# Kernel optimization log

Measured on AMD Instinct MI355X. Metric: run time of the kernel, lower is better.

Reference implementation:

```python
import jax, jax.numpy as jnp
import numpy as np

D = 768
H = 8
DH = D // H
SCALE = DH ** -0.5


def layer_norm(x, g, b, eps=1e-5):
    mu = jnp.mean(x, axis=-1, keepdims=True)
    var = jnp.var(x, axis=-1, keepdims=True)
    return (x - mu) * jax.lax.rsqrt(var + eps) * g + b


def setup_inputs() -> dict:
    key = jax.random.key(0)
    ks = jax.random.split(key, 8)
    B, N = 8, 1024
    s = lambda fan_in: 1.0 / np.sqrt(fan_in)
    return {
        "x": jax.random.normal(ks[0], (B, N, D), jnp.float32),
        "w_qkv": jax.random.normal(ks[1], (D, 3 * D), jnp.float32) * s(D),
        "w_o": jax.random.normal(ks[2], (D, D), jnp.float32) * s(D),
        "b_o": jnp.zeros((D,), jnp.float32),
        "w1": jax.random.normal(ks[3], (D, 4 * D), jnp.float32) * s(D),
        "b1": jnp.zeros((4 * D,), jnp.float32),
        "w2": jax.random.normal(ks[4], (4 * D, D), jnp.float32) * s(4 * D),
        "b2": jnp.zeros((D,), jnp.float32),
        "g1": jnp.ones((D,), jnp.float32), "be1": jnp.zeros((D,), jnp.float32),
        "gm": jnp.ones((D,), jnp.float32), "bm": jnp.zeros((D,), jnp.float32),
        "g3": jnp.ones((D,), jnp.float32), "be3": jnp.zeros((D,), jnp.float32),
    }


def reference(x, w_qkv, w_o, b_o, w1, b1, w2, b2, g1, be1, gm, bm, g3, be3):
    B, N, _ = x.shape
    # --- attention branch (pre-norm) ---
    h = layer_norm(x, g1, be1)
    qkv = h @ w_qkv                                   # (B,N,3D)
    qkv = qkv.reshape(B, N, 3, H, DH).transpose(2, 0, 3, 1, 4)  # (3,B,H,N,Dh)
    q, k, v = qkv[0], qkv[1], qkv[2]
    att = jax.nn.softmax(jnp.einsum('bhnd,bhmd->bhnm', q, k) * SCALE, axis=-1)
    o = jnp.einsum('bhnm,bhmd->bhnd', att, v)         # (B,H,N,Dh)
    # faithful to original: reshape WITHOUT transposing heads back
    o = o.reshape(B, N, D)
    o = o @ w_o + b_o
    x = o + x
    # --- MLP branch (has its own pre-norm; GELU after BOTH linears; dropout off) ---
    h = layer_norm(x, gm, bm)
    h = jax.nn.gelu(h @ w1 + b1, approximate=False)
    h = jax.nn.gelu(h @ w2 + b2, approximate=False)
    x = h + x
    return layer_norm(x, g3, be3)
```

## Files before the change

kernel.cpp:

```cpp
#include <hip/hip_runtime.h>
#include <cmath>
#include <cstdint>

typedef __bf16 bf16;
typedef __bf16 bf16x8 __attribute__((ext_vector_type(8)));
typedef __bf16 bf16x4 __attribute__((ext_vector_type(4)));
typedef float  f32x4  __attribute__((ext_vector_type(4)));

#define M_TOK 8192
#define SCALE_ 0.10206207261596575f

__device__ __forceinline__ void gld_lds16(const void* g, void* l) {
  __builtin_amdgcn_global_load_lds(
      (__attribute__((address_space(1))) void*)(uintptr_t)g,
      (__attribute__((address_space(3))) void*)(uintptr_t)l,
      16, 0, 0);
}

__device__ __forceinline__ float gelu_f(float x) {
  float u = x * (0.7978845608f + 0.0356774081f * x * x);
  float t = 1.0f - 2.0f / (__expf(2.0f * u) + 1.0f);
  return 0.5f * x * (1.0f + t);
}

__global__ __launch_bounds__(256) void make_frags_kernel(
    const float* __restrict__ w_qkv, const float* __restrict__ w_o,
    const float* __restrict__ w1, const float* __restrict__ w2,
    bf16* __restrict__ fqkv, bf16* __restrict__ fwo, bf16* __restrict__ fw1,
    bf16* __restrict__ fw2) {
  int chunk = blockIdx.x * 4 + (threadIdx.x >> 6);
  int lane = threadIdx.x & 63;
  const float* src;
  bf16* dst;
  int K, N, base;
  if (chunk < 3456) {
    src = w_qkv; dst = fqkv; K = 768; N = 2304; base = 0;
  } else if (chunk < 4608) {
    src = w_o; dst = fwo; K = 768; N = 768; base = 3456;
  } else if (chunk < 9216) {
    src = w1; dst = fw1; K = 768; N = 3072; base = 4608;
  } else {
    src = w2; dst = fw2; K = 3072; N = 768; base = 9216;
  }
  int lid = chunk - base;
  int kc = K / 32;
  int n16 = lid / kc, c = lid - n16 * kc;
  int lr = lane & 15, qd = lane >> 4;
  int n = n16 * 16 + lr;
  int k0 = c * 32 + qd * 8;
  bf16x8 v;
#pragma unroll
  for (int e = 0; e < 8; e++) v[e] = (bf16)src[(size_t)(k0 + e) * N + n];
  *(bf16x8*)&dst[(size_t)lid * 512 + lane * 8] = v;
}

__global__ __launch_bounds__(256) void ln_kernel(
    const float* __restrict__ x, const float* __restrict__ g,
    const float* __restrict__ b, bf16* __restrict__ ob) {
  int w = threadIdx.x >> 6, lane = threadIdx.x & 63;
  size_t row = (size_t)blockIdx.x * 4 + w;
  const float* xr = x + row * 768;
  float4 v[3];
  float s = 0.f, sq = 0.f;
#pragma unroll
  for (int k = 0; k < 3; k++) {
    v[k] = *(const float4*)(xr + (k * 64 + lane) * 4);
    s += v[k].x + v[k].y + v[k].z + v[k].w;
    sq += v[k].x * v[k].x + v[k].y * v[k].y + v[k].z * v[k].z + v[k].w * v[k].w;
  }
#pragma unroll
  for (int off = 32; off >= 1; off >>= 1) {
    s += __shfl_xor(s, off);
    sq += __shfl_xor(sq, off);
  }
  float mean = s * (1.f / 768.f);
  float rstd = rsqrtf(sq * (1.f / 768.f) - mean * mean + 1e-5f);
#pragma unroll
  for (int k = 0; k < 3; k++) {
    int c = (k * 64 + lane) * 4;
    float4 gg = *(const float4*)(g + c);
    float4 bb = *(const float4*)(b + c);
    bf16x4 pk = {(bf16)((v[k].x - mean) * rstd * gg.x + bb.x),
                 (bf16)((v[k].y - mean) * rstd * gg.y + bb.y),
                 (bf16)((v[k].z - mean) * rstd * gg.z + bb.z),
                 (bf16)((v[k].w - mean) * rstd * gg.w + bb.w)};
    *(bf16x4*)(ob + row * 768 + c) = pk;
  }
}

__global__ __launch_bounds__(256) void ln2_reduce_kernel(
    const bf16* __restrict__ p, const float* __restrict__ bo,
    const float* __restrict__ xres, const float* __restrict__ g,
    const float* __restrict__ b, bf16* __restrict__ x2,
    bf16* __restrict__ h2) {
  int w = threadIdx.x >> 6, lane = threadIdx.x & 63;
  size_t row = (size_t)blockIdx.x * 4 + w;
  const bf16* p0 = p + row * 768;
  const bf16* p1 = p0 + (size_t)M_TOK * 768;
  const float* xr = xres + row * 768;
  float4 v[3];
  float s = 0.f, sq = 0.f;
#pragma unroll
  for (int k = 0; k < 3; k++) {
    int c = (k * 64 + lane) * 4;
    bf16x4 a0 = *(const bf16x4*)(p0 + c);
    bf16x4 a1 = *(const bf16x4*)(p1 + c);
    float4 bb = *(const float4*)(bo + c);
    float4 rr = *(const float4*)(xr + c);
    v[k].x = (float)a0[0] + (float)a1[0] + bb.x + rr.x;
    v[k].y = (float)a0[1] + (float)a1[1] + bb.y + rr.y;
    v[k].z = (float)a0[2] + (float)a1[2] + bb.z + rr.z;
    v[k].w = (float)a0[3] + (float)a1[3] + bb.w + rr.w;
    bf16x4 xo = {(bf16)v[k].x, (bf16)v[k].y, (bf16)v[k].z, (bf16)v[k].w};
    *(bf16x4*)(x2 + row * 768 + c) = xo;
    s += v[k].x + v[k].y + v[k].z + v[k].w;
    sq += v[k].x * v[k].x + v[k].y * v[k].y + v[k].z * v[k].z + v[k].w * v[k].w;
  }
#pragma unroll
  for (int off = 32; off >= 1; off >>= 1) {
    s += __shfl_xor(s, off);
    sq += __shfl_xor(sq, off);
  }
  float mean = s * (1.f / 768.f);
  float rstd = rsqrtf(sq * (1.f / 768.f) - mean * mean + 1e-5f);
#pragma unroll
  for (int k = 0; k < 3; k++) {
    int c = (k * 64 + lane) * 4;
    float4 gg = *(const float4*)(g + c);
    float4 bb = *(const float4*)(b + c);
    bf16x4 pk = {(bf16)((v[k].x - mean) * rstd * gg.x + bb.x),
                 (bf16)((v[k].y - mean) * rstd * gg.y + bb.y),
                 (bf16)((v[k].z - mean) * rstd * gg.z + bb.z),
                 (bf16)((v[k].w - mean) * rstd * gg.w + bb.w)};
    *(bf16x4*)(h2 + row * 768 + c) = pk;
  }
}

__global__ __launch_bounds__(256) void ln3_reduce_kernel(
    const bf16* __restrict__ p, const float* __restrict__ b2,
    const bf16* __restrict__ x2, const float* __restrict__ g,
    const float* __restrict__ b, float* __restrict__ out) {
  int w = threadIdx.x >> 6, lane = threadIdx.x & 63;
  size_t row = (size_t)blockIdx.x * 4 + w;
  const bf16* p0 = p + row * 768;
  const bf16* p1 = p0 + (size_t)M_TOK * 768;
  const bf16* xr = x2 + row * 768;
  float4 v[3];
  float s = 0.f, sq = 0.f;
#pragma unroll
  for (int k = 0; k < 3; k++) {
    int c = (k * 64 + lane) * 4;
    bf16x4 a0 = *(const bf16x4*)(p0 + c);
    bf16x4 a1 = *(const bf16x4*)(p1 + c);
    float4 bb = *(const float4*)(b2 + c);
    bf16x4 rr = *(const bf16x4*)(xr + c);
    v[k].x = gelu_f((float)a0[0] + (float)a1[0] + bb.x) + (float)rr[0];
    v[k].y = gelu_f((float)a0[1] + (float)a1[1] + bb.y) + (float)rr[1];
    v[k].z = gelu_f((float)a0[2] + (float)a1[2] + bb.z) + (float)rr[2];
    v[k].w = gelu_f((float)a0[3] + (float)a1[3] + bb.w) + (float)rr[3];
    s += v[k].x + v[k].y + v[k].z + v[k].w;
    sq += v[k].x * v[k].x + v[k].y * v[k].y + v[k].z * v[k].z + v[k].w * v[k].w;
  }
#pragma unroll
  for (int off = 32; off >= 1; off >>= 1) {
    s += __shfl_xor(s, off);
    sq += __shfl_xor(sq, off);
  }
  float mean = s * (1.f / 768.f);
  float rstd = rsqrtf(sq * (1.f / 768.f) - mean * mean + 1e-5f);
#pragma unroll
  for (int k = 0; k < 3; k++) {
    int c = (k * 64 + lane) * 4;
    float4 gg = *(const float4*)(g + c);
    float4 bb = *(const float4*)(b + c);
    float4 ov = {(v[k].x - mean) * rstd * gg.x + bb.x,
                 (v[k].y - mean) * rstd * gg.y + bb.y,
                 (v[k].z - mean) * rstd * gg.z + bb.z,
                 (v[k].w - mean) * rstd * gg.w + bb.w};
    *(float4*)(out + row * 768 + c) = ov;
  }
}

template <int EPI, int LDA, int KTOT, int KSL, int NN>
__global__ __launch_bounds__(256, 3) void gemm128_kernel(
    const bf16* __restrict__ A, const bf16* __restrict__ Bf,
    const float* __restrict__ bias, bf16* __restrict__ outb,
    bf16* __restrict__ qo, bf16* __restrict__ ko, bf16* __restrict__ vto) {
  constexpr int KCg = KTOT / 32;
  constexpr int NT = KSL / 32;
  __shared__ __align__(16) bf16 smem[3][8192];
  int tid = threadIdx.x;
  int w = tid >> 6, l = tid & 63;
  int qd = l >> 4, lr = l & 15;
  int id2 = blockIdx.y * gridDim.x + blockIdx.x;
  int xcd = id2 & 7;
  int slot = id2 >> 3;
  int Mg = gridDim.x >> 3;
  int mt = xcd * Mg + (slot % Mg);
  int ntl = slot / Mg;
  int bm0 = mt * 128, bn0 = ntl * 128;
  int kb = blockIdx.z * KSL;
  int wm = (w >> 1) * 64, wn = (w & 1) * 64;
  int wnl = (w & 1) * 4;

  const bf16* pA = A + (size_t)(bm0 + w * 32 + (l >> 2)) * LDA + kb +
                   (((l & 3) ^ ((l >> 3) & 3)) * 8);
  const bf16* pB =
      Bf + ((size_t)((bn0 >> 4) + w * 2) * KCg + (kb >> 5)) * 512 + l * 8;

  auto STG = [&](int t, int b) {
    char* dA = (char*)smem[b] + w * 2048;
    char* dB = (char*)smem[b] + 8192 + w * 2048;
    gld_lds16(pA + t * 32, dA);
    gld_lds16(pA + t * 32 + (size_t)16 * LDA, dA + 1024);
    gld_lds16(pB + (size_t)t * 512, dB);
    gld_lds16(pB + (size_t)KCg * 512 + (size_t)t * 512, dB + 1024);
  };
  auto LDF = [&](int b, bf16x8* af, bf16x8* bv) {
    const bf16* Ab = smem[b];
    const bf16* Bb = smem[b] + 4096;
#pragma unroll
    for (int i = 0; i < 4; ++i) {
      int r = wm + i * 16 + lr;
      af[i] = *(const bf16x8*)(Ab + r * 32 + ((qd ^ ((lr >> 1) & 3)) * 8));
    }
#pragma unroll
    for (int j = 0; j < 4; ++j)
      bv[j] = *(const bf16x8*)(Bb + (wnl + j) * 512 + l * 8);
  };

  f32x4 acc[4][4] = {};

  STG(0, 0);
  STG(1, 1);
  asm volatile("s_waitcnt vmcnt(4)" ::: "memory");
  __builtin_amdgcn_sched_barrier(0);
  __builtin_amdgcn_s_barrier();

#pragma unroll 1
  for (int t3 = 0; t3 < NT; t3 += 3) {
#pragma unroll
    for (int u = 0; u < 3; ++u) {
      const int t = t3 + u;
      const bool st = (t + 2) < NT;
      if (st) STG(t + 2, (u + 2) % 3);
      __builtin_amdgcn_sched_barrier(0);
      bf16x8 af[4], bv[4];
      LDF(u, af, bv);
      asm volatile("s_waitcnt lgkmcnt(0)" ::: "memory");
      __builtin_amdgcn_sched_barrier(0);
      __builtin_amdgcn_s_setprio(1);
#pragma unroll
      for (int i = 0; i < 4; ++i)
#pragma unroll
        for (int j = 0; j < 4; ++j)
          acc[i][j] = __builtin_amdgcn_mfma_f32_16x16x32_bf16(
              af[i], bv[j], acc[i][j], 0, 0, 0);
      __builtin_amdgcn_s_setprio(0);
      if (t + 1 < NT) {
        if (st) asm volatile("s_waitcnt vmcnt(4)" ::: "memory");
        else    asm volatile("s_waitcnt vmcnt(0)" ::: "memory");
        __builtin_amdgcn_sched_barrier(0);
        __builtin_amdgcn_s_barrier();
      }
    }
  }

  bf16* outbs = (EPI == 5) ? outb + (size_t)blockIdx.z * M_TOK * NN : outb;

#pragma unroll
  for (int i = 0; i < 4; i++) {
#pragma unroll
    for (int j = 0; j < 4; j++) {
      if (EPI == 4) {
        int colt = bn0 + wn + j * 16;
        int which = colt / 768;
        int rem = colt - which * 768;
        int h = rem / 96;
        int dhb = rem - h * 96;
        int row0 = bm0 + wm + i * 16 + qd * 4;
        int b = row0 >> 10, n0 = row0 & 1023;
        int bh = b * 8 + h;
        if (which == 2) {
          bf16x4 pk = {(bf16)acc[i][j][0], (bf16)acc[i][j][1],
                       (bf16)acc[i][j][2], (bf16)acc[i][j][3]};
          *(bf16x4*)(vto + ((size_t)(bh * 96 + dhb + lr)) * 1024 + n0) = pk;
        } else if (which == 0) {
#pragma unroll
          for (int r = 0; r < 4; r++)
            qo[((size_t)bh * 1024 + n0 + r) * 96 + dhb + lr] =
                (bf16)(acc[i][j][r] * SCALE_);
        } else {
#pragma unroll
          for (int r = 0; r < 4; r++)
            ko[((size_t)bh * 1024 + n0 + r) * 96 + dhb + lr] =
                (bf16)acc[i][j][r];
        }
      } else {
#pragma unroll
        for (int r = 0; r < 4; r++) {
          int row = bm0 + wm + i * 16 + qd * 4 + r;
          int col = bn0 + wn + j * 16 + lr;
          size_t o = (size_t)row * NN + col;
          float v = acc[i][j][r];
          if (EPI == 2) {
            outbs[o] = (bf16)gelu_f(v + bias[col]);
          } else {
            outbs[o] = (bf16)v;
          }
        }
      }
    }
  }
}

__global__ __launch_bounds__(256) void attn_kernel(
    const bf16* __restrict__ qb, const bf16* __restrict__ kb,
    const bf16* __restrict__ vtb, bf16* __restrict__ operm) {
  __shared__ __align__(16) bf16 Ks[2][64 * 104];
  __shared__ __align__(16) bf16 Vs[2][96 * 72];
  __shared__ __align__(16) bf16 Ps[128 * 72];
  int t = threadIdx.x;
  int w = t >> 6, lane = t & 63;
  int qd = lane >> 4, lr = lane & 15;
  int bh = blockIdx.x, nt0 = blockIdx.y * 128;
  int bq = bh >> 3, hh = bh & 7;

  const bf16* kgb = kb + (size_t)bh * 1024 * 96;
  const bf16* vgb = vtb + (size_t)bh * 96 * 1024;

  bf16x8 kreg[3], vreg[3];
#pragma unroll
  for (int it = 0; it < 3; it++) {
    int idx = it * 256 + t;
    kreg[it] = *(const bf16x8*)(kgb + (idx / 12) * 96 + (idx % 12) * 8);
    vreg[it] = *(const bf16x8*)(vgb + (size_t)(idx >> 3) * 1024 + (idx & 7) * 8);
  }

  const bf16* qg = qb + ((size_t)bh * 1024 + nt0 + w * 32) * 96;
  bf16x8 afq[2][3];
#pragma unroll
  for (int i = 0; i < 2; i++)
#pragma unroll
    for (int ks = 0; ks < 3; ks++)
      afq[i][ks] = *(const bf16x8*)(qg + (i * 16 + lr) * 96 + ks * 32 + qd * 8);

  f32x4 oacc[2][6] = {};
  float lst[2][4] = {};

  int cur = 0;
  for (int kt = 0; kt < 16; kt++) {
#pragma unroll
    for (int it = 0; it < 3; it++) {
      int idx = it * 256 + t;
      *(bf16x8*)&Ks[cur][(idx / 12) * 104 + (idx % 12) * 8] = kreg[it];
      *(bf16x8*)&Vs[cur][(idx >> 3) * 72 + (idx & 7) * 8] = vreg[it];
    }
    if (kt < 15) {
      const bf16* kg = kgb + (size_t)(kt + 1) * 64 * 96;
      const bf16* vg = vgb + (kt + 1) * 64;
#pragma unroll
      for (int it = 0; it < 3; it++) {
        int idx = it * 256 + t;
        kreg[it] = *(const bf16x8*)(kg + (idx / 12) * 96 + (idx % 12) * 8);
        vreg[it] =
            *(const bf16x8*)(vg + (size_t)(idx >> 3) * 1024 + (idx & 7) * 8);
      }
    }
    __syncthreads();

    f32x4 sacc[2][4] = {};
#pragma unroll
    for (int ks = 0; ks < 3; ks++) {
      bf16x8 bk[4];
#pragma unroll
      for (int jn = 0; jn < 4; jn++)
        bk[jn] =
            *(const bf16x8*)&Ks[cur][(jn * 16 + lr) * 104 + ks * 32 + qd * 8];
#pragma unroll
      for (int i = 0; i < 2; i++)
#pragma unroll
        for (int jn = 0; jn < 4; jn++)
          sacc[i][jn] = __builtin_amdgcn_mfma_f32_16x16x32_bf16(
              afq[i][ks], bk[jn], sacc[i][jn], 0, 0, 0);
    }

#pragma unroll
    for (int i = 0; i < 2; i++)
#pragma unroll
      for (int jn = 0; jn < 4; jn++)
#pragma unroll
        for (int r = 0; r < 4; r++) {
          float p = __expf(sacc[i][jn][r]);
          lst[i][r] += p;
          Ps[(w * 32 + i * 16 + qd * 4 + r) * 72 + jn * 16 + lr] = (bf16)p;
        }

#pragma unroll
    for (int ks = 0; ks < 2; ks++) {
      bf16x8 ap[2];
#pragma unroll
      for (int i = 0; i < 2; i++)
        ap[i] =
            *(const bf16x8*)&Ps[(w * 32 + i * 16 + lr) * 72 + ks * 32 + qd * 8];
#pragma unroll
      for (int jn = 0; jn < 6; jn++) {
        bf16x8 bv =
            *(const bf16x8*)&Vs[cur][(jn * 16 + lr) * 72 + ks * 32 + qd * 8];
#pragma unroll
        for (int i = 0; i < 2; i++)
          oacc[i][jn] = __builtin_amdgcn_mfma_f32_16x16x32_bf16(
              ap[i], bv, oacc[i][jn], 0, 0, 0);
      }
    }
    cur ^= 1;
  }

#pragma unroll
  for (int i = 0; i < 2; i++)
#pragma unroll
    for (int r = 0; r < 4; r++) {
#pragma unroll
      for (int off = 1; off < 16; off <<= 1)
        lst[i][r] += __shfl_xor(lst[i][r], off);
    }

#pragma unroll
  for (int i = 0; i < 2; i++) {
#pragma unroll
    for (int r = 0; r < 4; r++) {
      float inv = 1.0f / lst[i][r];
      int n = nt0 + w * 32 + i * 16 + qd * 4 + r;
      size_t rowo = (size_t)bq * 1024 + hh * 128 + (n >> 3);
      int colb = 96 * (n & 7);
#pragma unroll
      for (int jn = 0; jn < 6; jn++)
        operm[rowo * 768 + colb + jn * 16 + lr] =
            (bf16)(oacc[i][jn][r] * inv);
    }
  }
}

extern "C" void kernel_launch(void* const* d_in, const int* in_sizes, int n_in,
                              void* d_out, int out_size, void* d_ws,
                              size_t ws_size, hipStream_t stream) {
  const float* x = (const float*)d_in[0];
  const float* w_qkv = (const float*)d_in[1];
  const float* w_o = (const float*)d_in[2];
  const float* b_o = (const float*)d_in[3];
  const float* w1 = (const float*)d_in[4];
  const float* b1 = (const float*)d_in[5];
  const float* w2 = (const float*)d_in[6];
  const float* b2 = (const float*)d_in[7];
  const float* g1 = (const float*)d_in[8];
  const float* be1 = (const float*)d_in[9];
  const float* gm = (const float*)d_in[10];
  const float* bm = (const float*)d_in[11];
  const float* g3 = (const float*)d_in[12];
  const float* be3 = (const float*)d_in[13];

  char* ws = (char*)d_ws;
  size_t off = 0;
  auto alloc = [&](size_t bytes) {
    char* p = ws + off;
    off += (bytes + 255) & ~(size_t)255;
    return p;
  };
  const size_t SZ_TOK_BF = (size_t)M_TOK * 768 * 2;
  bf16* fqkv = (bf16*)alloc((size_t)2304 * 768 * 2);
  bf16* fwo = (bf16*)alloc((size_t)768 * 768 * 2);
  bf16* fw1 = (bf16*)alloc((size_t)3072 * 768 * 2);
  bf16* fw2 = (bf16*)alloc((size_t)768 * 3072 * 2);
  bf16* hA = (bf16*)alloc(SZ_TOK_BF);
  bf16* qb = (bf16*)alloc(SZ_TOK_BF);
  bf16* kbuf = (bf16*)alloc(SZ_TOK_BF);
  bf16* vtb = (bf16*)alloc(SZ_TOK_BF);
  bf16* x2 = (bf16*)alloc(SZ_TOK_BF);
  char* G = alloc((size_t)M_TOK * 3072 * 2);
  bf16* operm = hA;
  bf16* h2 = hA;
  bf16* pWo = (bf16*)G;
  bf16* a1 = (bf16*)G;
  bf16* pW2 = hA;

  make_frags_kernel<<<3456, 256, 0, stream>>>(w_qkv, w_o, w1, w2, fqkv, fwo,
                                              fw1, fw2);

  ln_kernel<<<M_TOK / 4, 256, 0, stream>>>(x, g1, be1, hA);

  gemm128_kernel<4, 768, 768, 768, 2304><<<dim3(64, 18), 256, 0, stream>>>(
      hA, fqkv, nullptr, nullptr, qb, kbuf, vtb);

  attn_kernel<<<dim3(64, 8), 256, 0, stream>>>(qb, kbuf, vtb, operm);

  gemm128_kernel<5, 768, 768, 384, 768><<<dim3(64, 6, 2), 256, 0, stream>>>(
      operm, fwo, nullptr, pWo, nullptr, nullptr, nullptr);

  ln2_reduce_kernel<<<M_TOK / 4, 256, 0, stream>>>(pWo, b_o, x, gm, bm, x2, h2);

  gemm128_kernel<2, 768, 768, 768, 3072><<<dim3(64, 24), 256, 0, stream>>>(
      h2, fw1, b1, a1, nullptr, nullptr, nullptr);

  gemm128_kernel<5, 3072, 3072, 1536, 768><<<dim3(64, 6, 2), 256, 0, stream>>>(
      a1, fw2, nullptr, pW2, nullptr, nullptr, nullptr);

  ln3_reduce_kernel<<<M_TOK / 4, 256, 0, stream>>>(pW2, b2, x2, g3, be3,
                                                   (float*)d_out);
}
```

Baseline: 321.0 us.

## Add 256x256-tile 8-wave GEMM with ping-pong LDS pipeline for QKV and MLP

Adds a new GEMM kernel that uses 256x256 output tiles, 512 threads, a 64-wide K step and double-buffered 128KB LDS. Global-to-LDS staging is interleaved with MFMA sub-phases, and each sub-phase is separated by barriers. The QKV, MLP-up and MLP-down GEMMs move to this kernel, while the 128-tile kernel is kept only for the output projection. Larger tiles raise arithmetic intensity and cut redundant global loads. In exchange the grids are smaller (288/384/192 blocks at one block per CU), which risks tail effects and lower occupancy, and the many barriers add synchronisation cost.

```diff
diff --git a/kernel.cpp b/kernel.cpp
--- a/kernel.cpp
+++ b/kernel.cpp
@@ -9,6 +9,7 @@
 
 #define M_TOK 8192
 #define SCALE_ 0.10206207261596575f
+#define SB0 __builtin_amdgcn_sched_barrier(0)
 
 __device__ __forceinline__ void gld_lds16(const void* g, void* l) {
   __builtin_amdgcn_global_load_lds(
@@ -178,6 +179,196 @@
                  (v[k].z - mean) * rstd * gg.z + bb.z,
                  (v[k].w - mean) * rstd * gg.w + bb.w};
     *(float4*)(out + row * 768 + c) = ov;
+  }
+}
+
+template <int EPI, int LDA, int KTOT, int KSL, int NN>
+__global__ __launch_bounds__(512, 1) void gemm256_kernel(
+    const bf16* __restrict__ A, const bf16* __restrict__ Bf,
+    const float* __restrict__ bias, bf16* __restrict__ outb,
+    bf16* __restrict__ qo, bf16* __restrict__ ko, bf16* __restrict__ vto) {
+  constexpr int KCg = KTOT / 32;
+  constexpr int NT = KSL / 64;
+  constexpr int NI = NT / 2;
+  __shared__ __align__(16) bf16 smem[2][32768];
+  int tid = threadIdx.x;
+  int w = tid >> 6, l = tid & 63;
+  int qd = l >> 4, lr = l & 15;
+  int bm0 = blockIdx.x * 256, bn0 = blockIdx.y * 256;
+  int kb = blockIdx.z * KSL;
+  int wm = (w >> 2) * 128;
+  int wn = (w & 3) * 64;
+  int wnl = (w & 3) * 4;
+
+  const bf16* pA = A + (size_t)(bm0 + w * 32 + (l >> 2)) * LDA + kb +
+                   (((l & 3) ^ ((l >> 3) & 3)) * 8);
+  const bf16* pB =
+      Bf + ((size_t)((bn0 >> 4) + 2 * w) * KCg + (kb >> 5)) * 512 + l * 8;
+
+  auto STG_A = [&](int t, int kc, bf16* buf) {
+    const bf16* s = pA + t * 64 + kc * 32;
+    char* d = (char*)buf + kc * 16384 + w * 2048;
+    gld_lds16(s, d);
+    gld_lds16(s + (size_t)16 * LDA, d + 1024);
+  };
+  auto STG_B = [&](int t, int kc, bf16* buf) {
+    const bf16* s = pB + (size_t)(t * 2 + kc) * 512;
+    char* d = (char*)buf + 32768 + kc * 16384 + w * 2048;
+    gld_lds16(s, d);
+    gld_lds16(s + (size_t)KCg * 512, d + 1024);
+  };
+  auto LD_A4 = [&](const bf16* buf, int kc, int i0, bf16x8* af) {
+#pragma unroll
+    for (int i = 0; i < 4; ++i) {
+      int r = wm + (i0 + i) * 16 + lr;
+      af[i] = *(const bf16x8*)(buf + kc * 8192 + r * 32 +
+                               ((qd ^ ((lr >> 1) & 3)) * 8));
+    }
+  };
+  auto LD_B4 = [&](const bf16* buf, int kc, bf16x8* bv) {
+#pragma unroll
+    for (int j = 0; j < 4; ++j)
+      bv[j] = *(const bf16x8*)(buf + 16384 + kc * 8192 + (wnl + j) * 512 +
+                               l * 8);
+  };
+
+  f32x4 acc[8][4] = {};
+  auto MM = [&](bf16x8* af, bf16x8* bv, int i0) {
+#pragma unroll
+    for (int i = 0; i < 4; ++i)
+#pragma unroll
+      for (int j = 0; j < 4; ++j)
+        acc[i0 + i][j] = __builtin_amdgcn_mfma_f32_16x16x32_bf16(
+            af[i], bv[j], acc[i0 + i][j], 0, 0, 0);
+  };
+
+  bf16* b0 = smem[0];
+  bf16* b1 = smem[1];
+
+  STG_B(0, 0, b0); STG_A(0, 0, b0); STG_B(0, 1, b0); STG_A(0, 1, b0);
+  STG_B(1, 0, b1); STG_A(1, 0, b1); STG_B(1, 1, b1);
+  asm volatile("s_waitcnt vmcnt(6)" ::: "memory");
+  SB0;
+  __builtin_amdgcn_s_barrier();
+  SB0;
+
+  bf16x8 af[4], bv[4];
+
+#pragma unroll 1
+  for (int it = 0; it < NI; ++it) {
+    const int T = 2 * it;
+    const bool st = (it + 1 < NI);
+
+    SB0; LD_B4(b0, 0, bv); LD_A4(b0, 0, 0, af); SB0;
+    STG_A(T + 1, 1, b1);
+    SB0; __builtin_amdgcn_s_barrier();
+    asm volatile("s_waitcnt lgkmcnt(0)" ::: "memory"); SB0;
+    __builtin_amdgcn_s_setprio(1); MM(af, bv, 0); __builtin_amdgcn_s_setprio(0);
+    SB0; __builtin_amdgcn_s_barrier();
+
+    SB0; LD_A4(b0, 0, 4, af); SB0;
+    if (st) STG_B(T + 2, 0, b0);
+    SB0; __builtin_amdgcn_s_barrier();
+    asm volatile("s_waitcnt lgkmcnt(0)" ::: "memory"); SB0;
+    __builtin_amdgcn_s_setprio(1); MM(af, bv, 4); __builtin_amdgcn_s_setprio(0);
+    SB0; __builtin_amdgcn_s_barrier();
+
+    SB0; LD_B4(b0, 1, bv); LD_A4(b0, 1, 0, af); SB0;
+    if (st) STG_A(T + 2, 0, b0);
+    SB0; __builtin_amdgcn_s_barrier();
+    asm volatile("s_waitcnt lgkmcnt(0)" ::: "memory"); SB0;
+    __builtin_amdgcn_s_setprio(1); MM(af, bv, 0); __builtin_amdgcn_s_setprio(0);
+    SB0; __builtin_amdgcn_s_barrier();
+
+    SB0; LD_A4(b0, 1, 4, af); SB0;
+    if (st) STG_B(T + 2, 1, b0);
+    SB0; __builtin_amdgcn_s_barrier();
+    asm volatile("s_waitcnt lgkmcnt(0)" ::: "memory"); SB0;
+    __builtin_amdgcn_s_setprio(1); MM(af, bv, 4); __builtin_amdgcn_s_setprio(0);
+    SB0;
+    if (st) asm volatile("s_waitcnt vmcnt(6)" ::: "memory");
+    else    asm volatile("s_waitcnt vmcnt(0)" ::: "memory");
+    SB0; __builtin_amdgcn_s_barrier();
+
+    SB0; LD_B4(b1, 0, bv); LD_A4(b1, 0, 0, af); SB0;
+    if (st) STG_A(T + 2, 1, b0);
+    SB0; __builtin_amdgcn_s_barrier();
+    asm volatile("s_waitcnt lgkmcnt(0)" ::: "memory"); SB0;
+    __builtin_amdgcn_s_setprio(1); MM(af, bv, 0); __builtin_amdgcn_s_setprio(0);
+    SB0; __builtin_amdgcn_s_barrier();
+
+    SB0; LD_A4(b1, 0, 4, af); SB0;
+    if (st) STG_B(T + 3, 0, b1);
+    SB0; __builtin_amdgcn_s_barrier();
+    asm volatile("s_waitcnt lgkmcnt(0)" ::: "memory"); SB0;
+    __builtin_amdgcn_s_setprio(1); MM(af, bv, 4); __builtin_amdgcn_s_setprio(0);
+    SB0; __builtin_amdgcn_s_barrier();
+
+    SB0; LD_B4(b1, 1, bv); LD_A4(b1, 1, 0, af); SB0;
+    if (st) STG_A(T + 3, 0, b1);
+    SB0; __builtin_amdgcn_s_barrier();
+    asm volatile("s_waitcnt lgkmcnt(0)" ::: "memory"); SB0;
+    __builtin_amdgcn_s_setprio(1); MM(af, bv, 0); __builtin_amdgcn_s_setprio(0);
+    SB0; __builtin_amdgcn_s_barrier();
+
+    SB0; LD_A4(b1, 1, 4, af); SB0;
+    if (st) STG_B(T + 3, 1, b1);
+    SB0; __builtin_amdgcn_s_barrier();
+    asm volatile("s_waitcnt lgkmcnt(0)" ::: "memory"); SB0;
+    __builtin_amdgcn_s_setprio(1); MM(af, bv, 4); __builtin_amdgcn_s_setprio(0);
+    SB0;
+    if (st) {
+      asm volatile("s_waitcnt vmcnt(6)" ::: "memory");
+      SB0;
+      __builtin_amdgcn_s_barrier();
+    }
+  }
+
+  bf16* outbs = (EPI == 5) ? outb + (size_t)blockIdx.z * M_TOK * NN : outb;
+
+#pragma unroll
+  for (int i = 0; i < 8; i++) {
+#pragma unroll
+    for (int j = 0; j < 4; j++) {
+      if (EPI == 4) {
+        int colt = bn0 + wn + j * 16;
+        int which = colt / 768;
+        int rem = colt - which * 768;
+        int h = rem / 96;
+        int dhb = rem - h * 96;
+        int row0 = bm0 + wm + i * 16 + qd * 4;
+        int b = row0 >> 10, n0 = row0 & 1023;
+        int bh = b * 8 + h;
+        if (which == 2) {
+          bf16x4 pk = {(bf16)acc[i][j][0], (bf16)acc[i][j][1],
+                       (bf16)acc[i][j][2], (bf16)acc[i][j][3]};
+          *(bf16x4*)(vto + ((size_t)(bh * 96 + dhb + lr)) * 1024 + n0) = pk;
+        } else if (which == 0) {
+#pragma unroll
+          for (int r = 0; r < 4; r++)
+            qo[((size_t)bh * 1024 + n0 + r) * 96 + dhb + lr] =
+                (bf16)(acc[i][j][r] * SCALE_);
+        } else {
+#pragma unroll
+          for (int r = 0; r < 4; r++)
+            ko[((size_t)bh * 1024 + n0 + r) * 96 + dhb + lr] =
+                (bf16)acc[i][j][r];
+        }
+      } else {
+#pragma unroll
+        for (int r = 0; r < 4; r++) {
+          int row = bm0 + wm + i * 16 + qd * 4 + r;
+          int col = bn0 + wn + j * 16 + lr;
+          size_t o = (size_t)row * NN + col;
+          float v = acc[i][j][r];
+          if (EPI == 2) {
+            outbs[o] = (bf16)gelu_f(v + bias[col]);
+          } else {
+            outbs[o] = (bf16)v;
+          }
+        }
+      }
+    }
   }
 }
 
@@ -234,7 +425,7 @@
   STG(0, 0);
   STG(1, 1);
   asm volatile("s_waitcnt vmcnt(4)" ::: "memory");
-  __builtin_amdgcn_sched_barrier(0);
+  SB0;
   __builtin_amdgcn_s_barrier();
 
 #pragma unroll 1
@@ -244,11 +435,11 @@
       const int t = t3 + u;
       const bool st = (t + 2) < NT;
       if (st) STG(t + 2, (u + 2) % 3);
-      __builtin_amdgcn_sched_barrier(0);
+      SB0;
       bf16x8 af[4], bv[4];
       LDF(u, af, bv);
       asm volatile("s_waitcnt lgkmcnt(0)" ::: "memory");
-      __builtin_amdgcn_sched_barrier(0);
+      SB0;
       __builtin_amdgcn_s_setprio(1);
 #pragma unroll
       for (int i = 0; i < 4; ++i)
@@ -260,7 +451,7 @@
       if (t + 1 < NT) {
         if (st) asm volatile("s_waitcnt vmcnt(4)" ::: "memory");
         else    asm volatile("s_waitcnt vmcnt(0)" ::: "memory");
-        __builtin_amdgcn_sched_barrier(0);
+        SB0;
         __builtin_amdgcn_s_barrier();
       }
     }
@@ -272,42 +463,16 @@
   for (int i = 0; i < 4; i++) {
 #pragma unroll
     for (int j = 0; j < 4; j++) {
-      if (EPI == 4) {
-        int colt = bn0 + wn + j * 16;
-        int which = colt / 768;
-        int rem = colt - which * 768;
-        int h = rem / 96;
-        int dhb = rem - h * 96;
-        int row0 = bm0 + wm + i * 16 + qd * 4;
-        int b = row0 >> 10, n0 = row0 & 1023;
-        int bh = b * 8 + h;
-        if (which == 2) {
-          bf16x4 pk = {(bf16)acc[i][j][0], (bf16)acc[i][j][1],
-                       (bf16)acc[i][j][2], (bf16)acc[i][j][3]};
-          *(bf16x4*)(vto + ((size_t)(bh * 96 + dhb + lr)) * 1024 + n0) = pk;
-        } else if (which == 0) {
-#pragma unroll
-          for (int r = 0; r < 4; r++)
-            qo[((size_t)bh * 1024 + n0 + r) * 96 + dhb + lr] =
-                (bf16)(acc[i][j][r] * SCALE_);
+#pragma unroll
+      for (int r = 0; r < 4; r++) {
+        int row = bm0 + wm + i * 16 + qd * 4 + r;
+        int col = bn0 + wn + j * 16 + lr;
+        size_t o = (size_t)row * NN + col;
+        float v = acc[i][j][r];
+        if (EPI == 2) {
+          outbs[o] = (bf16)gelu_f(v + bias[col]);
         } else {
-#pragma unroll
-          for (int r = 0; r < 4; r++)
-            ko[((size_t)bh * 1024 + n0 + r) * 96 + dhb + lr] =
-                (bf16)acc[i][j][r];
-        }
-      } else {
-#pragma unroll
-        for (int r = 0; r < 4; r++) {
-          int row = bm0 + wm + i * 16 + qd * 4 + r;
-          int col = bn0 + wn + j * 16 + lr;
-          size_t o = (size_t)row * NN + col;
-          float v = acc[i][j][r];
-          if (EPI == 2) {
-            outbs[o] = (bf16)gelu_f(v + bias[col]);
-          } else {
-            outbs[o] = (bf16)v;
-          }
+          outbs[o] = (bf16)v;
         }
       }
     }
@@ -488,7 +653,7 @@
 
   ln_kernel<<<M_TOK / 4, 256, 0, stream>>>(x, g1, be1, hA);
 
-  gemm128_kernel<4, 768, 768, 768, 2304><<<dim3(64, 18), 256, 0, stream>>>(
+  gemm256_kernel<4, 768, 768, 768, 2304><<<dim3(32, 9), 512, 0, stream>>>(
       hA, fqkv, nullptr, nullptr, qb, kbuf, vtb);
 
   attn_kernel<<<dim3(64, 8), 256, 0, stream>>>(qb, kbuf, vtb, operm);
@@ -498,10 +663,10 @@
 
   ln2_reduce_kernel<<<M_TOK / 4, 256, 0, stream>>>(pWo, b_o, x, gm, bm, x2, h2);
 
-  gemm128_kernel<2, 768, 768, 768, 3072><<<dim3(64, 24), 256, 0, stream>>>(
+  gemm256_kernel<2, 768, 768, 768, 3072><<<dim3(32, 12), 512, 0, stream>>>(
       h2, fw1, b1, a1, nullptr, nullptr, nullptr);
 
-  gemm128_kernel<5, 3072, 3072, 1536, 768><<<dim3(64, 6, 2), 256, 0, stream>>>(
+  gemm256_kernel<5, 3072, 3072, 1536, 768><<<dim3(32, 3, 2), 512, 0, stream>>>(
       a1, fw2, nullptr, pW2, nullptr, nullptr, nullptr);
 
   ln3_reduce_kernel<<<M_TOK / 4, 256, 0, stream>>>(pW2, b2, x2, g3, be3,
```

Result: slower. 360.5 us (+12.3%).

## Fuse output projection, residual and LayerNorm into attention kernel epilogue

Applied to the files above, without the earlier changes.

The attention kernel now stages its normalized output for 16 permuted token rows in LDS. It multiplies them by the W_o fragments directly from global memory, then adds bias and residual and computes the MLP pre-norm, writing x2 and h2. This removes the split-K Wo GEMM, the partial-sum round trip and the separate LN2 reduce kernel. It also XOR-swizzles the P tile in LDS to reduce bank conflicts. In exchange each attention block streams all of W_o from global/L2 with no LDS reuse, which lengthens the attention kernel and may lower its occupancy.

```diff
diff --git a/kernel.cpp b/kernel.cpp
--- a/kernel.cpp
+++ b/kernel.cpp
@@ -9,6 +9,7 @@
 
 #define M_TOK 8192
 #define SCALE_ 0.10206207261596575f
+#define SB0 __builtin_amdgcn_sched_barrier(0)
 
 __device__ __forceinline__ void gld_lds16(const void* g, void* l) {
   __builtin_amdgcn_global_load_lds(
@@ -85,54 +86,6 @@
                  (bf16)((v[k].z - mean) * rstd * gg.z + bb.z),
                  (bf16)((v[k].w - mean) * rstd * gg.w + bb.w)};
     *(bf16x4*)(ob + row * 768 + c) = pk;
-  }
-}
-
-__global__ __launch_bounds__(256) void ln2_reduce_kernel(
-    const bf16* __restrict__ p, const float* __restrict__ bo,
-    const float* __restrict__ xres, const float* __restrict__ g,
-    const float* __restrict__ b, bf16* __restrict__ x2,
-    bf16* __restrict__ h2) {
-  int w = threadIdx.x >> 6, lane = threadIdx.x & 63;
-  size_t row = (size_t)blockIdx.x * 4 + w;
-  const bf16* p0 = p + row * 768;
-  const bf16* p1 = p0 + (size_t)M_TOK * 768;
-  const float* xr = xres + row * 768;
-  float4 v[3];
-  float s = 0.f, sq = 0.f;
-#pragma unroll
-  for (int k = 0; k < 3; k++) {
-    int c = (k * 64 + lane) * 4;
-    bf16x4 a0 = *(const bf16x4*)(p0 + c);
-    bf16x4 a1 = *(const bf16x4*)(p1 + c);
-    float4 bb = *(const float4*)(bo + c);
-    float4 rr = *(const float4*)(xr + c);
-    v[k].x = (float)a0[0] + (float)a1[0] + bb.x + rr.x;
-    v[k].y = (float)a0[1] + (float)a1[1] + bb.y + rr.y;
-    v[k].z = (float)a0[2] + (float)a1[2] + bb.z + rr.z;
-    v[k].w = (float)a0[3] + (float)a1[3] + bb.w + rr.w;
-    bf16x4 xo = {(bf16)v[k].x, (bf16)v[k].y, (bf16)v[k].z, (bf16)v[k].w};
-    *(bf16x4*)(x2 + row * 768 + c) = xo;
-    s += v[k].x + v[k].y + v[k].z + v[k].w;
-    sq += v[k].x * v[k].x + v[k].y * v[k].y + v[k].z * v[k].z + v[k].w * v[k].w;
-  }
-#pragma unroll
-  for (int off = 32; off >= 1; off >>= 1) {
-    s += __shfl_xor(s, off);
-    sq += __shfl_xor(sq, off);
-  }
-  float mean = s * (1.f / 768.f);
-  float rstd = rsqrtf(sq * (1.f / 768.f) - mean * mean + 1e-5f);
-#pragma unroll
-  for (int k = 0; k < 3; k++) {
-    int c = (k * 64 + lane) * 4;
-    float4 gg = *(const float4*)(g + c);
-    float4 bb = *(const float4*)(b + c);
-    bf16x4 pk = {(bf16)((v[k].x - mean) * rstd * gg.x + bb.x),
-                 (bf16)((v[k].y - mean) * rstd * gg.y + bb.y),
-                 (bf16)((v[k].z - mean) * rstd * gg.z + bb.z),
-                 (bf16)((v[k].w - mean) * rstd * gg.w + bb.w)};
-    *(bf16x4*)(h2 + row * 768 + c) = pk;
   }
 }
 
@@ -234,7 +187,7 @@
   STG(0, 0);
   STG(1, 1);
   asm volatile("s_waitcnt vmcnt(4)" ::: "memory");
-  __builtin_amdgcn_sched_barrier(0);
+  SB0;
   __builtin_amdgcn_s_barrier();
 
 #pragma unroll 1
@@ -244,11 +197,11 @@
       const int t = t3 + u;
       const bool st = (t + 2) < NT;
       if (st) STG(t + 2, (u + 2) % 3);
-      __builtin_amdgcn_sched_barrier(0);
+      SB0;
       bf16x8 af[4], bv[4];
       LDF(u, af, bv);
       asm volatile("s_waitcnt lgkmcnt(0)" ::: "memory");
-      __builtin_amdgcn_sched_barrier(0);
+      SB0;
       __builtin_amdgcn_s_setprio(1);
 #pragma unroll
       for (int i = 0; i < 4; ++i)
@@ -260,7 +213,7 @@
       if (t + 1 < NT) {
         if (st) asm volatile("s_waitcnt vmcnt(4)" ::: "memory");
         else    asm volatile("s_waitcnt vmcnt(0)" ::: "memory");
-        __builtin_amdgcn_sched_barrier(0);
+        SB0;
         __builtin_amdgcn_s_barrier();
       }
     }
@@ -316,7 +269,10 @@
 
 __global__ __launch_bounds__(256) void attn_kernel(
     const bf16* __restrict__ qb, const bf16* __restrict__ kb,
-    const bf16* __restrict__ vtb, bf16* __restrict__ operm) {
+    const bf16* __restrict__ vtb, const bf16* __restrict__ fwo,
+    const float* __restrict__ bo, const float* __restrict__ xres,
+    const float* __restrict__ gm, const float* __restrict__ bm,
+    bf16* __restrict__ x2o, bf16* __restrict__ h2o) {
   __shared__ __align__(16) bf16 Ks[2][64 * 104];
   __shared__ __align__(16) bf16 Vs[2][96 * 72];
   __shared__ __align__(16) bf16 Ps[128 * 72];
@@ -393,7 +349,8 @@
         for (int r = 0; r < 4; r++) {
           float p = __expf(sacc[i][jn][r]);
           lst[i][r] += p;
-          Ps[(w * 32 + i * 16 + qd * 4 + r) * 72 + jn * 16 + lr] = (bf16)p;
+          Ps[(w * 32 + i * 16 + qd * 4 + r) * 72 + ((jn ^ qd) * 16 + lr)] =
+              (bf16)p;
         }
 
 #pragma unroll
@@ -401,8 +358,9 @@
       bf16x8 ap[2];
 #pragma unroll
       for (int i = 0; i < 2; i++)
-        ap[i] =
-            *(const bf16x8*)&Ps[(w * 32 + i * 16 + lr) * 72 + ks * 32 + qd * 8];
+        ap[i] = *(const bf16x8*)&Ps[(w * 32 + i * 16 + lr) * 72 +
+                                    ((ks * 32 + qd * 8) ^
+                                     (((lr >> 2) & 3) * 16))];
 #pragma unroll
       for (int jn = 0; jn < 6; jn++) {
         bf16x8 bv =
@@ -425,18 +383,89 @@
         lst[i][r] += __shfl_xor(lst[i][r], off);
     }
 
+  bf16* Po = (bf16*)&Ks[0][0];
+  float* red = (float*)&Vs[0][0];
+  int Rbase = bq * 1024 + hh * 128 + (nt0 >> 3);
+
+  __syncthreads();
 #pragma unroll
   for (int i = 0; i < 2; i++) {
 #pragma unroll
     for (int r = 0; r < 4; r++) {
       float inv = 1.0f / lst[i][r];
-      int n = nt0 + w * 32 + i * 16 + qd * 4 + r;
-      size_t rowo = (size_t)bq * 1024 + hh * 128 + (n >> 3);
-      int colb = 96 * (n & 7);
+      int nn = i * 16 + qd * 4 + r;
+      int rloc = w * 4 + (nn >> 3);
+      int colb = 96 * (nn & 7);
 #pragma unroll
       for (int jn = 0; jn < 6; jn++)
-        operm[rowo * 768 + colb + jn * 16 + lr] =
-            (bf16)(oacc[i][jn][r] * inv);
+        Po[rloc * 784 + colb + jn * 16 + lr] = (bf16)(oacc[i][jn][r] * inv);
+    }
+  }
+  __syncthreads();
+
+  f32x4 ya[12] = {};
+#pragma unroll 1
+  for (int kc = 0; kc < 24; ++kc) {
+    bf16x8 a = *(const bf16x8*)&Po[lr * 784 + kc * 32 + qd * 8];
+    const bf16* bp = fwo + ((size_t)(w * 12) * 24 + kc) * 512 + lane * 8;
+#pragma unroll
+    for (int j = 0; j < 12; ++j)
+      ya[j] = __builtin_amdgcn_mfma_f32_16x16x32_bf16(
+          a, *(const bf16x8*)(bp + (size_t)j * 12288), ya[j], 0, 0, 0);
+  }
+
+  float s4[4] = {}, q4[4] = {};
+#pragma unroll
+  for (int j = 0; j < 12; ++j) {
+    int col = (w * 12 + j) * 16 + lr;
+    float bcol = bo[col];
+#pragma unroll
+    for (int rr = 0; rr < 4; ++rr) {
+      size_t R = (size_t)(Rbase + qd * 4 + rr);
+      float tv = ya[j][rr] + bcol + xres[R * 768 + col];
+      ya[j][rr] = tv;
+      s4[rr] += tv;
+      q4[rr] += tv * tv;
+    }
+  }
+#pragma unroll
+  for (int rr = 0; rr < 4; ++rr) {
+#pragma unroll
+    for (int off = 1; off < 16; off <<= 1) {
+      s4[rr] += __shfl_xor(s4[rr], off);
+      q4[rr] += __shfl_xor(q4[rr], off);
+    }
+  }
+  if (lr == 0) {
+#pragma unroll
+    for (int rr = 0; rr < 4; ++rr) {
+      red[(qd * 4 + rr) * 8 + w * 2] = s4[rr];
+      red[(qd * 4 + rr) * 8 + w * 2 + 1] = q4[rr];
+    }
+  }
+  __syncthreads();
+  float mean[4], rstd[4];
+#pragma unroll
+  for (int rr = 0; rr < 4; ++rr) {
+    float ss = 0.f, qq = 0.f;
+#pragma unroll
+    for (int wv = 0; wv < 4; ++wv) {
+      ss += red[(qd * 4 + rr) * 8 + wv * 2];
+      qq += red[(qd * 4 + rr) * 8 + wv * 2 + 1];
+    }
+    mean[rr] = ss * (1.f / 768.f);
+    rstd[rr] = rsqrtf(qq * (1.f / 768.f) - mean[rr] * mean[rr] + 1e-5f);
+  }
+#pragma unroll
+  for (int j = 0; j < 12; ++j) {
+    int col = (w * 12 + j) * 16 + lr;
+    float gg = gm[col], bb = bm[col];
+#pragma unroll
+    for (int rr = 0; rr < 4; ++rr) {
+      size_t R = (size_t)(Rbase + qd * 4 + rr);
+      float tv = ya[j][rr];
+      x2o[R * 768 + col] = (bf16)tv;
+      h2o[R * 768 + col] = (bf16)((tv - mean[rr]) * rstd[rr] * gg + bb);
     }
   }
 }
@@ -477,9 +506,7 @@
   bf16* vtb = (bf16*)alloc(SZ_TOK_BF);
   bf16* x2 = (bf16*)alloc(SZ_TOK_BF);
   char* G = alloc((size_t)M_TOK * 3072 * 2);
-  bf16* operm = hA;
   bf16* h2 = hA;
-  bf16* pWo = (bf16*)G;
   bf16* a1 = (bf16*)G;
   bf16* pW2 = hA;
 
@@ -491,12 +518,8 @@
   gemm128_kernel<4, 768, 768, 768, 2304><<<dim3(64, 18), 256, 0, stream>>>(
       hA, fqkv, nullptr, nullptr, qb, kbuf, vtb);
 
-  attn_kernel<<<dim3(64, 8), 256, 0, stream>>>(qb, kbuf, vtb, operm);
-
-  gemm128_kernel<5, 768, 768, 384, 768><<<dim3(64, 6, 2), 256, 0, stream>>>(
-      operm, fwo, nullptr, pWo, nullptr, nullptr, nullptr);
-
-  ln2_reduce_kernel<<<M_TOK / 4, 256, 0, stream>>>(pWo, b_o, x, gm, bm, x2, h2);
+  attn_kernel<<<dim3(64, 8), 256, 0, stream>>>(qb, kbuf, vtb, fwo, b_o, x, gm,
+                                               bm, x2, h2);
 
   gemm128_kernel<2, 768, 768, 768, 3072><<<dim3(64, 24), 256, 0, stream>>>(
       h2, fw1, b1, a1, nullptr, nullptr, nullptr);
```

After: 319.0 us (median of 2 runs). Within noise of the previous version (-0.6%).
